# Optimization experiments

Hardware: AMD Instinct MI355X
Metric: run time of the kernel (lower is better)

## Reference

```python
import jax, jax.numpy as jnp
import numpy as np

N = 50000      # nodes of type 'student'
E = 625000     # edges per relation
H = 128        # hidden_channels
C = 6          # num_classes
F_IN = 3       # hardcoded num_features in the module


def setup_inputs() -> dict:
    key = jax.random.key(0)
    ks = jax.random.split(key, 32)
    s = 0.05
    d = {}
    d["x_student"] = jax.random.normal(ks[0], (N, F_IN), dtype=jnp.float32)
    d["ei_friend"] = jax.random.randint(ks[1], (2, E), 0, N)
    d["ei_study"] = jax.random.randint(ks[2], (2, E), 0, N)
    # embedding Linear(3 -> H)
    d["emb_w"] = jax.random.normal(ks[3], (F_IN, H), dtype=jnp.float32) * s
    d["emb_b"] = jnp.zeros((H,), jnp.float32)
    # per-layer, per-edge-type RGCNConv params: relation-0 weight, root weight, bias
    i = 4
    for l in range(2):
        for e in ("f", "s"):
            d[f"w_rel_{l}_{e}"] = jax.random.normal(ks[i], (H, H), dtype=jnp.float32) * s; i += 1
            d[f"w_root_{l}_{e}"] = jax.random.normal(ks[i], (H, H), dtype=jnp.float32) * s; i += 1
            d[f"b_{l}_{e}"] = jnp.zeros((H,), jnp.float32)
    # output Linear(H -> C)
    d["out_w"] = jax.random.normal(ks[i], (H, C), dtype=jnp.float32) * s
    d["out_b"] = jnp.zeros((C,), jnp.float32)
    return d


def _rgcn_conv(h, ei, w_rel, w_root, b):
    # PyG RGCNConv with edge_type==0 everywhere: mean-aggregate src features at dst,
    # project by relation-0 weight, add root transform and bias.
    src, dst = ei[0], ei[1]
    msg = h[src]                                             # [E, H] gather
    agg = jax.ops.segment_sum(msg, dst, num_segments=N)      # [N, H]
    deg = jax.ops.segment_sum(jnp.ones((ei.shape[1],), h.dtype), dst, num_segments=N)
    agg = agg / jnp.maximum(deg, 1.0)[:, None]               # mean aggr (0 for isolated nodes)
    return agg @ w_rel + h @ w_root + b


def reference(x_student, ei_friend, ei_study, emb_w, emb_b,
              w_rel_0_f, w_root_0_f, b_0_f, w_rel_0_s, w_root_0_s, b_0_s,
              w_rel_1_f, w_root_1_f, b_1_f, w_rel_1_s, w_root_1_s, b_1_s,
              out_w, out_b):
    h = jax.nn.relu(x_student @ emb_w + emb_b)
    # layer 0: sum over the two relations, divide by valid_edge_count=2, relu (dropout eval=no-op)
    acc = _rgcn_conv(h, ei_friend, w_rel_0_f, w_root_0_f, b_0_f) \
        + _rgcn_conv(h, ei_study, w_rel_0_s, w_root_0_s, b_0_s)
    h = jax.nn.relu(acc / 2.0)
    # layer 1 (last): no relu/dropout
    acc = _rgcn_conv(h, ei_friend, w_rel_1_f, w_root_1_f, b_1_f) \
        + _rgcn_conv(h, ei_study, w_rel_1_s, w_root_1_s, b_1_s)
    h = acc / 2.0
    return h @ out_w + out_b
```

## Files before the change

### kernel.cpp

```cpp
#include <hip/hip_runtime.h>

#define NN 50000
#define NE 625000
#define HD 128
#define CAP 40
#define ZROW NN
#define WFL (12*8*64*8)
#define WFH (6*8*64*8)

typedef __attribute__((ext_vector_type(8))) short short8;
typedef __attribute__((ext_vector_type(4))) float f32x4;
typedef __attribute__((ext_vector_type(4))) unsigned uint4v;

__device__ __forceinline__ unsigned short f2bf(float f) {
    unsigned u = __builtin_bit_cast(unsigned, f);
    u += 0x7FFFu + ((u >> 16) & 1u);
    return (unsigned short)(u >> 16);
}
__device__ __forceinline__ unsigned pack2(float lo, float hi) {
    return (unsigned)f2bf(lo) | ((unsigned)f2bf(hi) << 16);
}
__device__ __forceinline__ float bflo(unsigned v) { unsigned u = v << 16; return __builtin_bit_cast(float, u); }
__device__ __forceinline__ float bfhi(unsigned v) { unsigned u = v & 0xFFFF0000u; return __builtin_bit_cast(float, u); }

__device__ __forceinline__ void extract8(uint4v u, int j0, int cnt, unsigned* out) {
    unsigned raw[8];
    raw[0] = u.x & 0xFFFFu; raw[1] = u.x >> 16;
    raw[2] = u.y & 0xFFFFu; raw[3] = u.y >> 16;
    raw[4] = u.z & 0xFFFFu; raw[5] = u.z >> 16;
    raw[6] = u.w & 0xFFFFu; raw[7] = u.w >> 16;
    #pragma unroll
    for (int j = 0; j < 8; ++j) out[j] = (j0 + j < cnt) ? raw[j] : ZROW;
}

__global__ __launch_bounds__(256) void k_prep(
    const float* __restrict__ x, const float* __restrict__ w,
    const float* __restrict__ b, unsigned* __restrict__ h0, unsigned* __restrict__ h1,
    const int* __restrict__ ei_f, const int* __restrict__ ei_s,
    int* __restrict__ degF, int* __restrict__ degS,
    unsigned short* __restrict__ bktF, unsigned short* __restrict__ bktS,
    const float* __restrict__ wrf0, const float* __restrict__ wtf0, const float* __restrict__ bf0,
    const float* __restrict__ wrs0, const float* __restrict__ wts0, const float* __restrict__ bs0,
    const float* __restrict__ wrf1, const float* __restrict__ wtf1, const float* __restrict__ bf1,
    const float* __restrict__ wrs1, const float* __restrict__ wts1, const float* __restrict__ bs1,
    unsigned short* __restrict__ Wf, float* __restrict__ bcat)
{
    int bid = blockIdx.x, t = threadIdx.x;
    if (bid < 3920) {
        int rel = bid >= 1960;
        int bqq = bid - rel * 1960;
        int cls = bqq & 7;
        int chunk = bqq >> 3;
        const int* ei; int* deg; unsigned short* bkt;
        if (rel == 0) { ei = ei_f; deg = degF; bkt = bktF; }
        else          { ei = ei_s; deg = degS; bkt = bktS; }
        const int lo = cls * 6250, hi = lo + 6250;
        int e0 = chunk * 2560 + t;
        #pragma unroll
        for (int i = 0; i < 10; ++i) {
            int e = e0 + i * 256;
            if (e >= NE) continue;
            int d = ei[NE + e];
            if (d >= lo && d < hi) {
                int s = ei[e];
                int pos = atomicAdd(&deg[d], 1);
                if (pos < CAP) bkt[d*CAP + pos] = (unsigned short)s;
            }
        }
    } else if (bid < 16420) {
        int i = (bid - 3920) * 256 + t;
        int n = i >> 6, c = (i & 63) * 2;
        float x0 = x[n*3+0], x1 = x[n*3+1], x2 = x[n*3+2];
        float v0 = fmaf(x0, w[c],   fmaf(x1, w[HD+c],   fmaf(x2, w[2*HD+c],   b[c])));
        float v1 = fmaf(x0, w[c+1], fmaf(x1, w[HD+c+1], fmaf(x2, w[2*HD+c+1], b[c+1])));
        v0 = fmaxf(v0, 0.f); v1 = fmaxf(v1, 0.f);
        h0[i] = pack2(v0, v1);
    } else if (bid == 16420) {
        if (t < 64)       h0[(long)ZROW*64 + t] = 0u;
        else if (t < 128) h1[(long)ZROW*64 + (t - 64)] = 0u;
    } else {
        int i = (bid - 16421) * 256 + t;
        int ln = i / 384, k = i - ln * 384;
        int l = ln >> 7, n = ln & 127;
        const float* wrf = l ? wrf1 : wrf0;
        const float* wrs = l ? wrs1 : wrs0;
        const float* wtf = l ? wtf1 : wtf0;
        const float* wts = l ? wts1 : wts0;
        float v;
        if (k < 128)      v = wrf[k*HD + n];
        else if (k < 256) v = wrs[(k-128)*HD + n];
        else              v = wtf[(k-256)*HD + n] + wts[(k-256)*HD + n];
        int nt = n >> 4, m16 = n & 15;
        int kc = k >> 5, rem = k & 31, quad = rem >> 3, j = rem & 7;
        int lane = quad * 16 + m16;
        Wf[(long)(((l*12 + kc)*8 + nt)*64 + lane)*8 + j] = f2bf(0.5f * v);
        if (i < 256) {
            int ll = i >> 7, cc = i & 127;
            const float* bfp = ll ? bf1 : bf0;
            const float* bsp = ll ? bs1 : bs0;
            bcat[i] = 0.5f * (bfp[cc] + bsp[cc]);
        }
    }
}

__global__ __launch_bounds__(256) void k_spmm(
    const unsigned* __restrict__ h,
    const int* __restrict__ degF, const int* __restrict__ degS,
    const unsigned short* __restrict__ bktF, const unsigned short* __restrict__ bktS,
    unsigned* __restrict__ aggF, unsigned* __restrict__ aggS)
{
    int w = threadIdx.x >> 6, lane = threadIdx.x & 63;
    int n = blockIdx.x * 4 + w;
    int dF = degF[n], dS = degS[n];
    int cF = min(dF, CAP), cS = min(dS, CAP);
    const unsigned short* rowF = bktF + (long)n*CAP;
    const unsigned short* rowS = bktS + (long)n*CAP;
    uint4v uF0 = *(const uint4v*)(rowF);
    uint4v uF1 = *(const uint4v*)(rowF + 8);
    uint4v uS0 = *(const uint4v*)(rowS);
    uint4v uS1 = *(const uint4v*)(rowS + 8);
    unsigned iF[16], iS[16];
    extract8(uF0, 0, cF, iF); extract8(uF1, 8, cF, iF + 8);
    extract8(uS0, 0, cS, iS); extract8(uS1, 8, cS, iS + 8);
    unsigned vF[16], vS[16];
    #pragma unroll
    for (int j = 0; j < 16; ++j) vF[j] = h[iF[j]*64u + lane];
    #pragma unroll
    for (int j = 0; j < 16; ++j) vS[j] = h[iS[j]*64u + lane];
    float aF0 = 0.f, aF1 = 0.f, aS0 = 0.f, aS1 = 0.f;
    #pragma unroll
    for (int j = 0; j < 16; ++j) { aF0 += bflo(vF[j]); aF1 += bfhi(vF[j]); }
    #pragma unroll
    for (int j = 0; j < 16; ++j) { aS0 += bflo(vS[j]); aS1 += bfhi(vS[j]); }
    for (int j = 16; j < cF; j += 8) {
        uint4v u = *(const uint4v*)(rowF + j);
        unsigned ii[8];
        extract8(u, j, cF, ii);
        unsigned vv[8];
        #pragma unroll
        for (int q = 0; q < 8; ++q) vv[q] = h[ii[q]*64u + lane];
        #pragma unroll
        for (int q = 0; q < 8; ++q) { aF0 += bflo(vv[q]); aF1 += bfhi(vv[q]); }
    }
    for (int j = 16; j < cS; j += 8) {
        uint4v u = *(const uint4v*)(rowS + j);
        unsigned ii[8];
        extract8(u, j, cS, ii);
        unsigned vv[8];
        #pragma unroll
        for (int q = 0; q < 8; ++q) vv[q] = h[ii[q]*64u + lane];
        #pragma unroll
        for (int q = 0; q < 8; ++q) { aS0 += bflo(vv[q]); aS1 += bfhi(vv[q]); }
    }
    float invF = 1.f / fmaxf((float)dF, 1.f);
    float invS = 1.f / fmaxf((float)dS, 1.f);
    aggF[n*64 + lane] = pack2(aF0*invF, aF1*invF);
    aggS[n*64 + lane] = pack2(aS0*invS, aS1*invS);
}

__global__ __launch_bounds__(256) void k_gemm(
    const unsigned short* __restrict__ A0, const unsigned short* __restrict__ A1,
    const unsigned short* __restrict__ A2,
    const unsigned short* __restrict__ Wf, const float* __restrict__ bias,
    unsigned short* __restrict__ outH, int mode,
    const float* __restrict__ ow, const float* __restrict__ ob,
    float* __restrict__ out6)
{
    __shared__ unsigned short Bs[WFH];
    const int t = threadIdx.x;
    const int wv = t >> 6, lane = t & 63;
    const int m16 = lane & 15, quad = lane >> 4;
    const int row0 = blockIdx.x * 64 + wv * 16;
    const int r = row0 + m16;
    const bool valid = r < NN;
    f32x4 acc[8];
    #pragma unroll
    for (int nt = 0; nt < 8; ++nt) acc[nt] = (f32x4){0.f,0.f,0.f,0.f};

    #pragma unroll
    for (int ph = 0; ph < 2; ++ph) {
        if (ph) __syncthreads();
        const uint4v* srcW = (const uint4v*)(Wf + (long)ph * WFH);
        uint4v* dstW = (uint4v*)Bs;
        #pragma unroll
        for (int i = 0; i < 12; ++i)
            dstW[i*256 + t] = srcW[i*256 + t];
        __syncthreads();
        #pragma unroll
        for (int kl = 0; kl < 6; ++kl) {
            int kc = ph*6 + kl;
            const unsigned short* src; int kofs;
            if (kc < 4)      { src = A0; kofs = kc*32; }
            else if (kc < 8) { src = A1; kofs = kc*32 - 128; }
            else             { src = A2; kofs = kc*32 - 256; }
            short8 a;
            if (valid) a = *(const short8*)(src + (long)r*HD + kofs + quad*8);
            else       a = short8{0,0,0,0,0,0,0,0};
            #pragma unroll
            for (int nt = 0; nt < 8; ++nt) {
                short8 bfr = *(const short8*)(Bs + ((kl*8 + nt)*64 + lane)*8);
                acc[nt] = __builtin_amdgcn_mfma_f32_16x16x32_bf16(a, bfr, acc[nt], 0, 0, 0);
            }
        }
    }

    float bs[8];
    #pragma unroll
    for (int nt = 0; nt < 8; ++nt) bs[nt] = bias[nt*16 + m16];

    if (mode == 0) {
        #pragma unroll
        for (int reg = 0; reg < 4; ++reg) {
            int rr = row0 + quad*4 + reg;
            if (rr >= NN) continue;
            #pragma unroll
            for (int nt = 0; nt < 8; ++nt) {
                float v = fmaxf(acc[nt][reg] + bs[nt], 0.f);
                outH[(long)rr*HD + nt*16 + m16] = f2bf(v);
            }
        }
    } else {
        float owr[8][6];
        #pragma unroll
        for (int nt = 0; nt < 8; ++nt) {
            int c = nt*16 + m16;
            #pragma unroll
            for (int j = 0; j < 6; ++j) owr[nt][j] = ow[c*6 + j];
        }
        #pragma unroll
        for (int reg = 0; reg < 4; ++reg) {
            int rr = row0 + quad*4 + reg;
            float tj[6] = {0,0,0,0,0,0};
            #pragma unroll
            for (int nt = 0; nt < 8; ++nt) {
                float hv = acc[nt][reg] + bs[nt];
                #pragma unroll
                for (int j = 0; j < 6; ++j) tj[j] = fmaf(hv, owr[nt][j], tj[j]);
            }
            #pragma unroll
            for (int mask = 1; mask < 16; mask <<= 1)
                #pragma unroll
                for (int j = 0; j < 6; ++j) tj[j] += __shfl_xor(tj[j], mask, 64);
            if (m16 == 0 && rr < NN) {
                #pragma unroll
                for (int j = 0; j < 6; ++j) out6[(long)rr*6 + j] = tj[j] + ob[j];
            }
        }
    }
}

extern "C" void kernel_launch(void* const* d_in, const int* in_sizes, int n_in,
                              void* d_out, int out_size, void* d_ws, size_t ws_size,
                              hipStream_t stream)
{
    const float* x     = (const float*)d_in[0];
    const int*   ei_f  = (const int*)d_in[1];
    const int*   ei_s  = (const int*)d_in[2];
    const float* emb_w = (const float*)d_in[3];
    const float* emb_b = (const float*)d_in[4];
    const float* wr0f  = (const float*)d_in[5];
    const float* wt0f  = (const float*)d_in[6];
    const float* b0f   = (const float*)d_in[7];
    const float* wr0s  = (const float*)d_in[8];
    const float* wt0s  = (const float*)d_in[9];
    const float* b0s   = (const float*)d_in[10];
    const float* wr1f  = (const float*)d_in[11];
    const float* wt1f  = (const float*)d_in[12];
    const float* b1f   = (const float*)d_in[13];
    const float* wr1s  = (const float*)d_in[14];
    const float* wt1s  = (const float*)d_in[15];
    const float* b1s   = (const float*)d_in[16];
    const float* out_w = (const float*)d_in[17];
    const float* out_b = (const float*)d_in[18];
    float* out = (float*)d_out;

    char* ws = (char*)d_ws;
    size_t off = 0;
    auto alloc = [&](size_t bytes) { char* p = ws + off; off += (bytes + 255) & ~255ULL; return p; };
    unsigned* h0   = (unsigned*)alloc((size_t)(NN+1)*64*4);
    unsigned* h1   = (unsigned*)alloc((size_t)(NN+1)*64*4);
    unsigned* aggF = (unsigned*)alloc((size_t)NN*64*4);
    unsigned* aggS = (unsigned*)alloc((size_t)NN*64*4);
    int*   degF = (int*)alloc((size_t)NN*4);
    int*   degS = (int*)alloc((size_t)NN*4);
    unsigned short* bktF = (unsigned short*)alloc((size_t)NN*CAP*2);
    unsigned short* bktS = (unsigned short*)alloc((size_t)NN*CAP*2);
    unsigned short* Wf = (unsigned short*)alloc((size_t)2*WFL*2);
    float* bcat = (float*)alloc((size_t)2*HD*4);

    hipMemsetAsync(degF, 0, ((NN*4 + 255) & ~255ULL) + NN*4, stream);

    k_prep<<<16805, 256, 0, stream>>>(x, emb_w, emb_b, h0, h1,
                                      ei_f, ei_s, degF, degS, bktF, bktS,
                                      wr0f, wt0f, b0f, wr0s, wt0s, b0s,
                                      wr1f, wt1f, b1f, wr1s, wt1s, b1s,
                                      Wf, bcat);
    k_spmm<<<NN/4, 256, 0, stream>>>(h0, degF, degS, bktF, bktS, aggF, aggS);
    k_gemm<<<(NN + 63)/64, 256, 0, stream>>>((const unsigned short*)aggF, (const unsigned short*)aggS,
                                             (const unsigned short*)h0, Wf, bcat,
                                             (unsigned short*)h1, 0, out_w, out_b, out);
    k_spmm<<<NN/4, 256, 0, stream>>>(h1, degF, degS, bktF, bktS, aggF, aggS);
    k_gemm<<<(NN + 63)/64, 256, 0, stream>>>((const unsigned short*)aggF, (const unsigned short*)aggS,
                                             (const unsigned short*)h1, Wf + WFL, bcat + HD,
                                             (unsigned short*)h1, 1, out_w, out_b, out);
}
```

Baseline: 274.6 us.

## Replace 8x edge rescans with two-pass binning before bucket fill

Edge bucketing used to have each of 8 destination-range classes rescan the whole edge list, which read the edge arrays eight times. It now runs a first pass that reads each edge once and appends a packed (local dst, src) word to a per-class bin, using a block-local histogram and a global cursor. A second kernel then walks each bin and does the per-node atomic bucket fill, keeping the locality of working on one destination range at a time. This adds a kernel launch, an intermediate bin buffer with a fixed capacity that silently drops overflow, and shared-memory atomics in the first pass.

New measurement: 276.4 us. No clear change (+0.6%).

```diff
diff --git a/kernel.cpp b/kernel.cpp
--- a/kernel.cpp
+++ b/kernel.cpp
@@ -7,6 +7,8 @@
 #define ZROW NN
 #define WFL (12*8*64*8)
 #define WFH (6*8*64*8)
+#define DPC 6250
+#define BINCAP 80000
 
 typedef __attribute__((ext_vector_type(8))) short short8;
 typedef __attribute__((ext_vector_type(4))) float f32x4;
@@ -33,53 +35,64 @@
     for (int j = 0; j < 8; ++j) out[j] = (j0 + j < cnt) ? raw[j] : ZROW;
 }
 
-__global__ __launch_bounds__(256) void k_prep(
+__global__ __launch_bounds__(256) void k_p1(
     const float* __restrict__ x, const float* __restrict__ w,
     const float* __restrict__ b, unsigned* __restrict__ h0, unsigned* __restrict__ h1,
     const int* __restrict__ ei_f, const int* __restrict__ ei_s,
-    int* __restrict__ degF, int* __restrict__ degS,
-    unsigned short* __restrict__ bktF, unsigned short* __restrict__ bktS,
+    int* __restrict__ cursor, unsigned* __restrict__ bin,
     const float* __restrict__ wrf0, const float* __restrict__ wtf0, const float* __restrict__ bf0,
     const float* __restrict__ wrs0, const float* __restrict__ wts0, const float* __restrict__ bs0,
     const float* __restrict__ wrf1, const float* __restrict__ wtf1, const float* __restrict__ bf1,
     const float* __restrict__ wrs1, const float* __restrict__ wts1, const float* __restrict__ bs1,
     unsigned short* __restrict__ Wf, float* __restrict__ bcat)
 {
+    __shared__ int hist[8], base[8], ofs[8];
     int bid = blockIdx.x, t = threadIdx.x;
-    if (bid < 3920) {
-        int rel = bid >= 1960;
-        int bqq = bid - rel * 1960;
-        int cls = bqq & 7;
-        int chunk = bqq >> 3;
-        const int* ei; int* deg; unsigned short* bkt;
-        if (rel == 0) { ei = ei_f; deg = degF; bkt = bktF; }
-        else          { ei = ei_s; deg = degS; bkt = bktS; }
-        const int lo = cls * 6250, hi = lo + 6250;
+    if (bid < 490) {
+        int rel = bid >= 245;
+        int chunk = bid - rel * 245;
+        const int* ei = rel ? ei_s : ei_f;
+        if (t < 8) { hist[t] = 0; ofs[t] = 0; }
+        __syncthreads();
+        int cls[10], dloc[10], srcv[10];
         int e0 = chunk * 2560 + t;
         #pragma unroll
         for (int i = 0; i < 10; ++i) {
             int e = e0 + i * 256;
-            if (e >= NE) continue;
-            int d = ei[NE + e];
-            if (d >= lo && d < hi) {
+            if (e < NE) {
+                int d = ei[NE + e];
                 int s = ei[e];
-                int pos = atomicAdd(&deg[d], 1);
-                if (pos < CAP) bkt[d*CAP + pos] = (unsigned short)s;
-            }
-        }
-    } else if (bid < 16420) {
-        int i = (bid - 3920) * 256 + t;
+                int c = d / DPC;
+                cls[i] = c; dloc[i] = d - c * DPC; srcv[i] = s;
+                atomicAdd(&hist[c], 1);
+            } else cls[i] = -1;
+        }
+        __syncthreads();
+        if (t < 8) base[t] = atomicAdd(&cursor[rel * 8 + t], hist[t]);
+        __syncthreads();
+        #pragma unroll
+        for (int i = 0; i < 10; ++i) {
+            if (cls[i] >= 0) {
+                int p = atomicAdd(&ofs[cls[i]], 1);
+                unsigned idx = (unsigned)(base[cls[i]] + p);
+                if (idx < BINCAP)
+                    bin[(long)(rel * 8 + cls[i]) * BINCAP + idx] =
+                        ((unsigned)dloc[i] << 16) | (unsigned)srcv[i];
+            }
+        }
+    } else if (bid < 12990) {
+        int i = (bid - 490) * 256 + t;
         int n = i >> 6, c = (i & 63) * 2;
         float x0 = x[n*3+0], x1 = x[n*3+1], x2 = x[n*3+2];
         float v0 = fmaf(x0, w[c],   fmaf(x1, w[HD+c],   fmaf(x2, w[2*HD+c],   b[c])));
         float v1 = fmaf(x0, w[c+1], fmaf(x1, w[HD+c+1], fmaf(x2, w[2*HD+c+1], b[c+1])));
         v0 = fmaxf(v0, 0.f); v1 = fmaxf(v1, 0.f);
         h0[i] = pack2(v0, v1);
-    } else if (bid == 16420) {
+    } else if (bid == 12990) {
         if (t < 64)       h0[(long)ZROW*64 + t] = 0u;
         else if (t < 128) h1[(long)ZROW*64 + (t - 64)] = 0u;
     } else {
-        int i = (bid - 16421) * 256 + t;
+        int i = (bid - 12991) * 256 + t;
         int ln = i / 384, k = i - ln * 384;
         int l = ln >> 7, n = ln & 127;
         const float* wrf = l ? wrf1 : wrf0;
@@ -99,6 +112,35 @@
             const float* bfp = ll ? bf1 : bf0;
             const float* bsp = ll ? bs1 : bs0;
             bcat[i] = 0.5f * (bfp[cc] + bsp[cc]);
+        }
+    }
+}
+
+__global__ __launch_bounds__(256) void k_p2(
+    const int* __restrict__ cursor, const unsigned* __restrict__ bin,
+    int* __restrict__ degF, int* __restrict__ degS,
+    unsigned short* __restrict__ bktF, unsigned short* __restrict__ bktS)
+{
+    int bid = blockIdx.x, t = threadIdx.x;
+    int rel = bid >= 504;
+    int bq = bid - rel * 504;
+    int cls = bq & 7;
+    int chunk = bq >> 3;
+    int cnt = min(cursor[rel * 8 + cls], BINCAP);
+    const unsigned* bp = bin + (long)(rel * 8 + cls) * BINCAP;
+    int* deg = rel ? degS : degF;
+    unsigned short* bkt = rel ? bktS : bktF;
+    const int dbase = cls * DPC;
+    int e0 = chunk * 1280 + t;
+    #pragma unroll
+    for (int i = 0; i < 5; ++i) {
+        int e = e0 + i * 256;
+        if (e < cnt) {
+            unsigned en = bp[e];
+            int src = en & 0xFFFFu;
+            int dst = dbase + (int)(en >> 16);
+            int pos = atomicAdd(&deg[dst], 1);
+            if (pos < CAP) bkt[(long)dst * CAP + pos] = (unsigned short)src;
         }
     }
 }
@@ -283,18 +325,22 @@
     unsigned* aggS = (unsigned*)alloc((size_t)NN*64*4);
     int*   degF = (int*)alloc((size_t)NN*4);
     int*   degS = (int*)alloc((size_t)NN*4);
+    int*   cursor = (int*)alloc((size_t)16*4);
     unsigned short* bktF = (unsigned short*)alloc((size_t)NN*CAP*2);
     unsigned short* bktS = (unsigned short*)alloc((size_t)NN*CAP*2);
     unsigned short* Wf = (unsigned short*)alloc((size_t)2*WFL*2);
     float* bcat = (float*)alloc((size_t)2*HD*4);
-
-    hipMemsetAsync(degF, 0, ((NN*4 + 255) & ~255ULL) + NN*4, stream);
-
-    k_prep<<<16805, 256, 0, stream>>>(x, emb_w, emb_b, h0, h1,
-                                      ei_f, ei_s, degF, degS, bktF, bktS,
-                                      wr0f, wt0f, b0f, wr0s, wt0s, b0s,
-                                      wr1f, wt1f, b1f, wr1s, wt1s, b1s,
-                                      Wf, bcat);
+    unsigned* bin = (unsigned*)alloc((size_t)16*BINCAP*4);
+
+    size_t degpad = ((size_t)NN*4 + 255) & ~255ULL;
+    hipMemsetAsync(degF, 0, degpad*2 + 64, stream);
+
+    k_p1<<<13375, 256, 0, stream>>>(x, emb_w, emb_b, h0, h1,
+                                    ei_f, ei_s, cursor, bin,
+                                    wr0f, wt0f, b0f, wr0s, wt0s, b0s,
+                                    wr1f, wt1f, b1f, wr1s, wt1s, b1s,
+                                    Wf, bcat);
+    k_p2<<<1008, 256, 0, stream>>>(cursor, bin, degF, degS, bktF, bktS);
     k_spmm<<<NN/4, 256, 0, stream>>>(h0, degF, degS, bktF, bktS, aggF, aggS);
     k_gemm<<<(NN + 63)/64, 256, 0, stream>>>((const unsigned short*)aggF, (const unsigned short*)aggS,
                                              (const unsigned short*)h0, Wf, bcat,
```
